# Performance work log

Hardware: AMD Instinct MI355X
Metric: run time of the kernel (lower is better)

## Reference

```python
import jax, jax.numpy as jnp
import numpy as np

B, DIM, N = 4, 256, 2048
DIM_CTX, M = 256, 2048
HEADS, DIM_HEAD = 8, 64
DIM_INNER = HEADS * DIM_HEAD  # 512
EPS = 1e-12  # matches F.normalize eps


def setup_inputs() -> dict:
    key = jax.random.key(0)
    ks = jax.random.split(key, 8)
    return {
        "fmap": jax.random.normal(ks[0], (B, DIM, N), dtype=jnp.float32),
        "context": jax.random.normal(ks[1], (B, DIM_CTX, M), dtype=jnp.float32),
        "mask": jax.random.randint(ks[2], (B, M), 0, 2) > 0,
        "gamma": jnp.ones((DIM, 1), dtype=jnp.float32),
        "gamma_ctx": jnp.ones((DIM_CTX, 1), dtype=jnp.float32),
        "Wq": jax.random.normal(ks[3], (DIM_INNER, DIM), dtype=jnp.float32) * (DIM ** -0.5),
        "Wkv": jax.random.normal(ks[4], (2 * DIM_INNER, DIM_CTX), dtype=jnp.float32) * (DIM_CTX ** -0.5),
        "Wout": jax.random.normal(ks[5], (DIM, DIM_INNER), dtype=jnp.float32) * (DIM_INNER ** -0.5),
    }


def channel_rmsnorm(x, gamma):
    # F.normalize(x, dim=1) * sqrt(dim) * gamma ; x: [b, c, n], gamma: [c, 1]
    scale = x.shape[1] ** 0.5
    norm = jnp.sqrt(jnp.sum(x * x, axis=1, keepdims=True))
    normed = x / jnp.maximum(norm, EPS)
    return normed * scale * gamma[None]


def reference(fmap, context, mask, gamma, gamma_ctx, Wq, Wkv, Wout):
    h, d = HEADS, DIM_HEAD
    attn_scale = d ** -0.5

    fmap_n = channel_rmsnorm(fmap, gamma)          # [b, dim, n]
    ctx_n = channel_rmsnorm(context, gamma_ctx)    # [b, dim_ctx, m]

    # 1x1 Conv1d == matmul over channels
    q = jnp.einsum('oc,bcn->bon', Wq, fmap_n)      # [b, h*d, n]
    kv = jnp.einsum('oc,bcm->bom', Wkv, ctx_n)     # [b, 2*h*d, m]
    k, v = jnp.split(kv, 2, axis=1)

    # [b, h*d, n] -> [b, h, n, d]
    def to_heads(t):
        b, _, nn = t.shape
        return t.reshape(b, h, d, nn).transpose(0, 1, 3, 2)

    q, k, v = to_heads(q), to_heads(k), to_heads(v)

    # L2-distance attention: sim = -||q_i - k_j||_2 * scale
    q2 = jnp.sum(q * q, axis=-1)                   # [b, h, n]
    k2 = jnp.sum(k * k, axis=-1)                   # [b, h, m]
    qk = jnp.einsum('bhid,bhjd->bhij', q, k)       # [b, h, n, m]
    d2 = jnp.maximum(q2[..., :, None] + k2[..., None, :] - 2.0 * qk, 0.0)
    dist = jnp.sqrt(jnp.maximum(d2, EPS))
    sim = -dist * attn_scale

    neg_max = -jnp.finfo(sim.dtype).max
    sim = jnp.where(mask[:, None, None, :], sim, neg_max)

    attn = jax.nn.softmax(sim, axis=-1)            # [b, h, n, m]
    out = jnp.einsum('bhij,bhjd->bhid', attn, v)   # [b, h, n, d]
    out = out.transpose(0, 1, 3, 2).reshape(out.shape[0], h * d, -1)  # [b, h*d, n]
    return jnp.einsum('oc,bcn->bon', Wout, out)    # [b, dim, n]
```

## Files before the change

kernel.cpp:

```cpp
#include <hip/hip_runtime.h>
#include <hip/hip_bf16.h>

#define B_ 4
#define DIM_ 256
#define N_ 2048
#define M_ 2048
#define HEADS_ 8
#define DHEAD_ 64
#define DINNER_ 512

typedef __attribute__((ext_vector_type(8))) short short8;
typedef __attribute__((ext_vector_type(4))) short short4v;
typedef __attribute__((ext_vector_type(4))) float floatx4;
typedef __attribute__((ext_vector_type(4))) _Float16 half4;
typedef __attribute__((ext_vector_type(8))) _Float16 half8;

#if defined(__has_builtin)
#if __has_builtin(__builtin_amdgcn_global_load_lds)
#define HAS_DMA 1
#endif
#endif

typedef __attribute__((address_space(1))) const void gvoid_t;
typedef __attribute__((address_space(3))) void lvoid_t;

#define CQ_ 0.18033688011112042f
#define NEG2CQ_ (-0.36067376022224084f)
#define EPS2_ 3.25213893e-14f

__device__ inline short bf16r(float x) {
  unsigned u = __float_as_uint(x);
  unsigned r = (u + 0x7fffu + ((u >> 16) & 1u)) >> 16;
  return (short)r;
}
__device__ inline float bf2f(short b) {
  return __uint_as_float(((unsigned)(unsigned short)b) << 16);
}

__global__ __launch_bounds__(256) void wsplit_kernel(
    const float* __restrict__ Wq, const float* __restrict__ Wkv,
    const float* __restrict__ Wout, const float* __restrict__ gamma,
    const float* __restrict__ gctx, short* __restrict__ whi,
    short* __restrict__ wlo) {
  const int y = blockIdx.y;
  const int gsz[3] = {32768, 65536, 32768};
  const int goff[3] = {0, 131072, 393216};
  int gidx = blockIdx.x * 256 + threadIdx.x;
  if (gidx >= gsz[y]) return;
  const float* W = (y == 0) ? Wq : (y == 1) ? Wkv : Wout;
  const int cmask = (y == 2) ? 511 : 255;
  int e0 = gidx * 4;
  int c = e0 & cmask;
  float4 wv = *(const float4*)&W[e0];
  if (y < 2) {
    const float* g = (y == 0) ? gamma : gctx;
    float4 g4 = *(const float4*)&g[c];
    wv.x *= g4.x; wv.y *= g4.y; wv.z *= g4.z; wv.w *= g4.w;
  }
  float vv[4] = {wv.x, wv.y, wv.z, wv.w};
  short4v hi, lo;
#pragma unroll
  for (int e = 0; e < 4; ++e) {
    short hb = bf16r(vv[e]);
    hi[e] = hb;
    lo[e] = bf16r(vv[e] - bf2f(hb));
  }
  *(short4v*)&whi[goff[y] + e0] = hi;
  *(short4v*)&wlo[goff[y] + e0] = lo;
}

__global__ __launch_bounds__(256) void colnorm_t_kernel(
    const float* __restrict__ xf, const float* __restrict__ xc,
    short* __restrict__ xtf, short* __restrict__ xtc, int NN) {
  const float* x = (blockIdx.z == 0) ? xf : xc;
  short* xt = (blockIdx.z == 0) ? xtf : xtc;
  int b = blockIdx.y;
  int tx = threadIdx.x, ty = threadIdx.y;
  int n0 = blockIdx.x * 64, n = n0 + tx;
  const float* xb = x + (size_t)b * 256 * NN;

  float ssq = 0.f;
  for (int c = ty; c < 256; c += 4) {
    float v = xb[(size_t)c * NN + n];
    ssq += v * v;
  }
  __shared__ float red[4][64];
  __shared__ float scl[64];
  __shared__ float t[64][65];
  red[ty][tx] = ssq;
  __syncthreads();
  if (ty == 0) {
    float s = red[0][tx] + red[1][tx] + red[2][tx] + red[3][tx];
    scl[tx] = 16.0f / fmaxf(sqrtf(s), 1e-12f);
  }
  int tid = ty * 64 + tx;
  int row = tid >> 2, cg = tid & 3;
  for (int c0 = 0; c0 < 256; c0 += 64) {
    __syncthreads();
    for (int cc = ty; cc < 64; cc += 4) t[cc][tx] = xb[(size_t)(c0 + cc) * NN + n];
    __syncthreads();
    float sc = scl[row];
    short8 o0v, o1v;
#pragma unroll
    for (int e = 0; e < 8; ++e) {
      o0v[e] = bf16r(t[cg * 16 + e][row] * sc);
      o1v[e] = bf16r(t[cg * 16 + 8 + e][row] * sc);
    }
    size_t base = ((size_t)b * NN + n0 + row) * 256 + c0 + cg * 16;
    *(short8*)&xt[base] = o0v;
    *(short8*)&xt[base + 8] = o1v;
  }
}

__global__ __launch_bounds__(256) void qkv_gemm_kernel(
    const short* __restrict__ whi, const short* __restrict__ wlo,
    const short* __restrict__ fmap_t, const short* __restrict__ ctx_t,
    short* __restrict__ qb, short* __restrict__ kc, _Float16* __restrict__ vc,
    const int* __restrict__ maskp, float* __restrict__ k2m) {
  const int b = blockIdx.z;
  const int y = blockIdx.y;
  const bool isq = (y < 4);
  const int o0 = (isq ? y : y - 4) * 128;
  const int n0 = blockIdx.x * 128;
  const short* Wh = whi + (isq ? 0 : 131072);
  const short* Wl = wlo + (isq ? 0 : 131072);
  const short* Xt = isq ? fmap_t : ctx_t;

  const int tid = threadIdx.x;
  const int w = tid >> 6, l = tid & 63, quad = l >> 4, l15 = l & 15;
  const int wo = (w >> 1) * 64, wn = (w & 1) * 64;

  __shared__ __align__(16) short Wa[2][128][40];
  __shared__ __align__(16) short Xb[128][40];

  floatx4 acc[4][4];
#pragma unroll
  for (int ot = 0; ot < 4; ++ot)
#pragma unroll
    for (int nt = 0; nt < 4; ++nt)
#pragma unroll
      for (int r = 0; r < 4; ++r) acc[ot][nt][r] = 0.f;

  for (int c0 = 0; c0 < 256; c0 += 32) {
    __syncthreads();
#pragma unroll
    for (int it = 0; it < 2; ++it) {
      int lin = tid + it * 256;
      int row = lin >> 2, sg = (lin & 3) * 8;
      size_t src = (size_t)(o0 + row) * 256 + c0 + sg;
      *(short8*)&Wa[0][row][sg] = *(const short8*)&Wh[src];
      *(short8*)&Wa[1][row][sg] = *(const short8*)&Wl[src];
    }
#pragma unroll
    for (int it = 0; it < 2; ++it) {
      int lin = tid + it * 256;
      int nn = lin >> 2, sg = (lin & 3) * 8;
      *(short8*)&Xb[nn][sg] =
          *(const short8*)&Xt[((size_t)b * 2048 + n0 + nn) * 256 + c0 + sg];
    }
    __syncthreads();

    short8 ah[4], al[4], bx[4];
#pragma unroll
    for (int ot = 0; ot < 4; ++ot) {
      ah[ot] = *(const short8*)&Wa[0][wo + 16 * ot + l15][8 * quad];
      al[ot] = *(const short8*)&Wa[1][wo + 16 * ot + l15][8 * quad];
    }
#pragma unroll
    for (int nt = 0; nt < 4; ++nt)
      bx[nt] = *(const short8*)&Xb[wn + 16 * nt + l15][8 * quad];
#pragma unroll
    for (int ot = 0; ot < 4; ++ot)
#pragma unroll
      for (int nt = 0; nt < 4; ++nt) {
        acc[ot][nt] =
            __builtin_amdgcn_mfma_f32_16x16x32_bf16(al[ot], bx[nt], acc[ot][nt], 0, 0, 0);
        acc[ot][nt] =
            __builtin_amdgcn_mfma_f32_16x16x32_bf16(ah[ot], bx[nt], acc[ot][nt], 0, 0, 0);
      }
  }

  if (isq) {
#pragma unroll
    for (int nt = 0; nt < 4; ++nt) {
      int n = n0 + wn + 16 * nt + l15;
      size_t base = ((size_t)b * 2048 + n) * 512;
#pragma unroll
      for (int ot = 0; ot < 4; ++ot) {
        int o = o0 + wo + 16 * ot + 4 * quad;
        short4v pk;
#pragma unroll
        for (int r = 0; r < 4; ++r) pk[r] = bf16r(CQ_ * acc[ot][nt][r]);
        *(short4v*)&qb[base + o] = pk;
      }
    }
  } else if (o0 < 512) {
    const int head = (o0 + wo) >> 6;
    const int bh = b * 8 + head;
    float k2p[4] = {0.f, 0.f, 0.f, 0.f};
#pragma unroll
    for (int nt = 0; nt < 4; ++nt) {
      int m = n0 + wn + 16 * nt + l15;
      int chunk = m >> 6, mrow = m & 63;
      size_t tbase = (((size_t)bh * 32 + chunk) * 64 + mrow) * 64;
      int sw = mrow & 7;
#pragma unroll
      for (int ot = 0; ot < 4; ++ot) {
        int d0 = 16 * ot + 4 * quad;
        short4v pk;
#pragma unroll
        for (int r = 0; r < 4; ++r) {
          short pv = bf16r(NEG2CQ_ * acc[ot][nt][r]);
          pk[r] = pv;
          float kr = bf2f(pv);
          k2p[nt] += kr * kr;
        }
        *(short4v*)&kc[tbase + (size_t)(((d0 >> 3) ^ sw) << 3) + (d0 & 7)] = pk;
      }
    }
#pragma unroll
    for (int nt = 0; nt < 4; ++nt) {
      float s = k2p[nt];
      s += __shfl_xor(s, 16);
      s += __shfl_xor(s, 32);
      if (quad == 0) {
        int m = n0 + wn + 16 * nt + l15;
        int mv = maskp[b * 2048 + m];
        k2m[(size_t)bh * 2048 + m] = mv ? 0.25f * s : __builtin_inff();
      }
    }
  } else {
    const int chv = o0 - 512 + wo;
    const int bh = b * 8 + (chv >> 6);
#pragma unroll
    for (int nt = 0; nt < 4; ++nt) {
      int j = n0 + wn + 16 * nt + l15;
      int chunk = j >> 6, jr = j & 63;
      int jrem = jr & 31;
      int colp = 32 * (jr >> 5) + ((jrem >> 2) & 3) * 8 + (jrem >> 4) * 4 +
                 (jrem & 3);
      size_t cbase = ((size_t)bh * 32 + chunk) * 4096;
#pragma unroll
      for (int ot = 0; ot < 4; ++ot)
#pragma unroll
        for (int r = 0; r < 4; ++r) {
          int drow = (chv + 16 * ot + 4 * quad + r) & 63;
          vc[cbase + drow * 64 + (((colp >> 3) ^ (drow & 7)) << 3) +
             (colp & 7)] = (_Float16)acc[ot][nt][r];
        }
    }
  }
}

__global__ __launch_bounds__(512, 8) void attn_kernel(
    const short* __restrict__ qb, const short* __restrict__ kc,
    const _Float16* __restrict__ vc, const float* __restrict__ k2m,
    short* __restrict__ attn_t) {
  const int bid = blockIdx.x;
  const int rr = bid & 7, qq = bid >> 3;
  const int bh = rr * 4 + (qq >> 5);
  const int iblk = qq & 31;
  const int h = bh & 7, b = bh >> 3;
  const int i0 = iblk * 64;

  const int tid = threadIdx.x;
  const int w = tid >> 6, l = tid & 63, quad = l >> 4, l15 = l & 15;
  const int wr = w >> 1, jh = w & 1;

  __shared__ __align__(16) short sbuf[2][2][4096];

  const short* qrow =
      qb + ((size_t)b * 2048 + i0 + 16 * wr + l15) * 512 + h * 64;
  const short* kcb = kc + (size_t)bh * 32 * 4096;
  const _Float16* vcb = vc + (size_t)bh * 32 * 4096;
  const float* k2b = k2m + (size_t)bh * 2048;

  short8 qa0 = *(const short8*)&qrow[8 * quad];
  short8 qa1 = *(const short8*)&qrow[32 + 8 * quad];
  float q2p = 0.f;
#pragma unroll
  for (int jj = 0; jj < 8; ++jj) {
    float f0 = bf2f(qa0[jj]), f1 = bf2f(qa1[jj]);
    q2p += f0 * f0 + f1 * f1;
  }
  q2p += __shfl_xor(q2p, 16);
  q2p += __shfl_xor(q2p, 32);
  const float q2c = q2p;

  floatx4 accO[4];
#pragma unroll
  for (int dt = 0; dt < 4; ++dt)
#pragma unroll
    for (int r = 0; r < 4; ++r) accO[dt][r] = 0.f;
  float lsum = 0.f;

  const int sx = l15 & 7;

  auto stage = [&](int c, int p) {
    const short* ks = kcb + (size_t)c * 4096 + w * 512 + l * 8;
    const _Float16* vs = vcb + (size_t)c * 4096 + w * 512 + l * 8;
#ifdef HAS_DMA
    __builtin_amdgcn_global_load_lds((gvoid_t*)ks,
                                     (lvoid_t*)&sbuf[0][p][w * 512], 16, 0, 0);
    __builtin_amdgcn_global_load_lds((gvoid_t*)vs,
                                     (lvoid_t*)&sbuf[1][p][w * 512], 16, 0, 0);
#else
    *(short8*)&sbuf[0][p][w * 512 + l * 8] = *(const short8*)ks;
    *(half8*)&((_Float16*)sbuf[1][p])[w * 512 + l * 8] = *(const half8*)vs;
#endif
  };

  stage(0, 0);
  for (int c = 0; c < 32; ++c) {
    __syncthreads();
    if (c < 31) stage(c + 1, (c + 1) & 1);
    const int p = c & 1;

    half4 pb0, pb1;
#pragma unroll
    for (int jt = 0; jt < 2; ++jt) {
      float4 k2v = *(const float4*)&k2b[c * 64 + jh * 32 + 16 * jt + 4 * quad];
      const short* kr = &sbuf[0][p][(jh * 32 + 16 * jt + l15) * 64];
      short8 k0 = *(const short8*)&kr[(quad ^ sx) << 3];
      short8 k1 = *(const short8*)&kr[((quad + 4) ^ sx) << 3];
      floatx4 a;
      a[0] = q2c + k2v.x;
      a[1] = q2c + k2v.y;
      a[2] = q2c + k2v.z;
      a[3] = q2c + k2v.w;
      __builtin_amdgcn_s_setprio(1);
      a = __builtin_amdgcn_mfma_f32_16x16x32_bf16(k0, qa0, a, 0, 0, 0);
      a = __builtin_amdgcn_mfma_f32_16x16x32_bf16(k1, qa1, a, 0, 0, 0);
      __builtin_amdgcn_s_setprio(0);
      half4 pbt;
#pragma unroll
      for (int r = 0; r < 4; ++r) {
        float s = __builtin_amdgcn_sqrtf(fmaxf(a[r], EPS2_));
        float pv = __builtin_amdgcn_exp2f(-s);
        lsum += pv;
        pbt[r] = (_Float16)pv;
      }
      if (jt == 0) pb0 = pbt; else pb1 = pbt;
    }

    __builtin_amdgcn_s_setprio(1);
#pragma unroll
    for (int dt = 0; dt < 4; ++dt) {
      const _Float16* vr = (const _Float16*)&sbuf[1][p][(16 * dt + l15) * 64];
      half8 hh = *(const half8*)&vr[((quad + 4 * jh) ^ sx) << 3];
      half4 vaA = __builtin_shufflevector(hh, hh, 0, 1, 2, 3);
      half4 vaB = __builtin_shufflevector(hh, hh, 4, 5, 6, 7);
      accO[dt] = __builtin_amdgcn_mfma_f32_16x16x16f16(vaA, pb0, accO[dt], 0, 0, 0);
      accO[dt] = __builtin_amdgcn_mfma_f32_16x16x16f16(vaB, pb1, accO[dt], 0, 0, 0);
    }
    __builtin_amdgcn_s_setprio(0);
  }

  __syncthreads();
  float* scr = (float*)sbuf;
  const int sidx = (wr * 64 + l) * 17;
  if (jh) {
#pragma unroll
    for (int dt = 0; dt < 4; ++dt)
#pragma unroll
      for (int r = 0; r < 4; ++r) scr[sidx + dt * 4 + r] = accO[dt][r];
    scr[sidx + 16] = lsum;
  }
  __syncthreads();
  if (!jh) {
#pragma unroll
    for (int dt = 0; dt < 4; ++dt)
#pragma unroll
      for (int r = 0; r < 4; ++r) accO[dt][r] += scr[sidx + dt * 4 + r];
    lsum += scr[sidx + 16];
    lsum += __shfl_xor(lsum, 16);
    lsum += __shfl_xor(lsum, 32);
    float rl = 1.0f / lsum;
    size_t base = ((size_t)b * 2048 + i0 + 16 * wr + l15) * 512 + h * 64;
#pragma unroll
    for (int dt = 0; dt < 4; ++dt) {
      short4v pk;
#pragma unroll
      for (int r = 0; r < 4; ++r) pk[r] = bf16r(accO[dt][r] * rl);
      *(short4v*)&attn_t[base + 16 * dt + 4 * quad] = pk;
    }
  }
}

__global__ __launch_bounds__(256) void outproj_kernel(
    const short* __restrict__ whi, const short* __restrict__ wlo,
    const short* __restrict__ Xt, float* __restrict__ Yf) {
  const int b = blockIdx.z;
  const int n0 = blockIdx.x * 128;
  const int o0 = blockIdx.y * 64;
  const int tid = threadIdx.x;
  const int w = tid >> 6, l = tid & 63, quad = l >> 4, l15 = l & 15;
  const int wo = (w >> 1) * 32, wn = (w & 1) * 64;

  __shared__ __align__(16) short Wa[2][64][40];
  __shared__ __align__(16) short Xb[128][40];

  floatx4 acc[2][4];
#pragma unroll
  for (int ot = 0; ot < 2; ++ot)
#pragma unroll
    for (int nt = 0; nt < 4; ++nt)
#pragma unroll
      for (int r = 0; r < 4; ++r) acc[ot][nt][r] = 0.f;

  for (int c0 = 0; c0 < 512; c0 += 32) {
    __syncthreads();
    {
      int row = tid >> 2, sg = (tid & 3) * 8;
      size_t src = (size_t)(o0 + row) * 512 + c0 + sg;
      *(short8*)&Wa[0][row][sg] = *(const short8*)&whi[src];
      *(short8*)&Wa[1][row][sg] = *(const short8*)&wlo[src];
    }
#pragma unroll
    for (int it = 0; it < 2; ++it) {
      int lin = tid + it * 256;
      int nn = lin >> 2, sg = (lin & 3) * 8;
      *(short8*)&Xb[nn][sg] =
          *(const short8*)&Xt[((size_t)b * 2048 + n0 + nn) * 512 + c0 + sg];
    }
    __syncthreads();

    short8 ah[2], al[2], bx[4];
#pragma unroll
    for (int ot = 0; ot < 2; ++ot) {
      ah[ot] = *(const short8*)&Wa[0][wo + 16 * ot + l15][8 * quad];
      al[ot] = *(const short8*)&Wa[1][wo + 16 * ot + l15][8 * quad];
    }
#pragma unroll
    for (int nt = 0; nt < 4; ++nt)
      bx[nt] = *(const short8*)&Xb[wn + 16 * nt + l15][8 * quad];
#pragma unroll
    for (int ot = 0; ot < 2; ++ot)
#pragma unroll
      for (int nt = 0; nt < 4; ++nt) {
        acc[ot][nt] =
            __builtin_amdgcn_mfma_f32_16x16x32_bf16(al[ot], bx[nt], acc[ot][nt], 0, 0, 0);
        acc[ot][nt] =
            __builtin_amdgcn_mfma_f32_16x16x32_bf16(ah[ot], bx[nt], acc[ot][nt], 0, 0, 0);
      }
  }

#pragma unroll
  for (int ot = 0; ot < 2; ++ot)
#pragma unroll
    for (int r = 0; r < 4; ++r) {
      int o = o0 + wo + 16 * ot + 4 * quad + r;
#pragma unroll
      for (int nt = 0; nt < 4; ++nt)
        Yf[((size_t)b * 256 + o) * 2048 + n0 + wn + 16 * nt + l15] =
            acc[ot][nt][r];
    }
}

extern "C" void kernel_launch(void* const* d_in, const int* in_sizes, int n_in,
                              void* d_out, int out_size, void* d_ws,
                              size_t ws_size, hipStream_t stream) {
  const float* fmap = (const float*)d_in[0];
  const float* context = (const float*)d_in[1];
  const int* mask = (const int*)d_in[2];
  const float* gamma = (const float*)d_in[3];
  const float* gamma_ctx = (const float*)d_in[4];
  const float* Wq = (const float*)d_in[5];
  const float* Wkv = (const float*)d_in[6];
  const float* Wout = (const float*)d_in[7];
  float* out = (float*)d_out;

  char* ws = (char*)d_ws;
  short* fmap_t = (short*)ws;
  short* ctx_t = fmap_t + 2097152;
  short* qb = ctx_t + 2097152;
  short* kc = qb + 4194304;
  _Float16* vc = (_Float16*)(kc + 4194304);
  short* attn_t = (short*)(vc + 4194304);
  float* k2m = (float*)(attn_t + 4194304);
  short* whi = (short*)(k2m + 65536);
  short* wlo = whi + 524288;

  dim3 blk64x4(64, 4);
  wsplit_kernel<<<dim3(256, 3), 256, 0, stream>>>(Wq, Wkv, Wout, gamma,
                                                  gamma_ctx, whi, wlo);
  colnorm_t_kernel<<<dim3(32, B_, 2), blk64x4, 0, stream>>>(
      fmap, context, fmap_t, ctx_t, N_);
  qkv_gemm_kernel<<<dim3(16, 12, B_), 256, 0, stream>>>(
      whi, wlo, fmap_t, ctx_t, qb, kc, vc, mask, k2m);
  attn_kernel<<<dim3(1024), 512, 0, stream>>>(qb, kc, vc, k2m, attn_t);
  outproj_kernel<<<dim3(16, 4, B_), 256, 0, stream>>>(whi + 393216,
                                                      wlo + 393216, attn_t,
                                                      out);
}
```

Before: 209.6 us.

## Software-pipeline attention loop: overlap P·V of previous tile with QK of current

Restructures the attention main loop so that the P·V MFMAs for the previous key tile run in the same iteration as the QK MFMAs for the current tile. The softmax probabilities are carried across iterations, and V staging is delayed by one stage. The change also prefetches the k2 norms one tile ahead in registers, and merges the two 16x16x16 f16 MFMAs into a single 16x16x32 f16 MFMA. The intent is to hide the sqrt/exp latency and LDS waits behind independent matrix work. In exchange it adds register pressure and an epilogue step for the final tile.

```diff
diff --git a/kernel.cpp b/kernel.cpp
--- a/kernel.cpp
+++ b/kernel.cpp
@@ -267,7 +267,8 @@
   const int w = tid >> 6, l = tid & 63, quad = l >> 4, l15 = l & 15;
   const int wr = w >> 1, jh = w & 1;
 
-  __shared__ __align__(16) short sbuf[2][2][4096];
+  __shared__ __align__(16) short kbuf[2][4096];
+  __shared__ __align__(16) short vbuf[2][4096];
 
   const short* qrow =
       qb + ((size_t)b * 2048 + i0 + 16 * wr + l15) * 512 + h * 64;
@@ -292,87 +293,120 @@
   for (int dt = 0; dt < 4; ++dt)
 #pragma unroll
     for (int r = 0; r < 4; ++r) accO[dt][r] = 0.f;
-  float lsum = 0.f;
+  float lsum0 = 0.f, lsum1 = 0.f;
 
   const int sx = l15 & 7;
 
-  auto stage = [&](int c, int p) {
+  auto stageK = [&](int c, int p) {
     const short* ks = kcb + (size_t)c * 4096 + w * 512 + l * 8;
+#ifdef HAS_DMA
+    __builtin_amdgcn_global_load_lds((gvoid_t*)ks,
+                                     (lvoid_t*)&kbuf[p][w * 512], 16, 0, 0);
+#else
+    *(short8*)&kbuf[p][w * 512 + l * 8] = *(const short8*)ks;
+#endif
+  };
+  auto stageV = [&](int c, int p) {
     const _Float16* vs = vcb + (size_t)c * 4096 + w * 512 + l * 8;
 #ifdef HAS_DMA
-    __builtin_amdgcn_global_load_lds((gvoid_t*)ks,
-                                     (lvoid_t*)&sbuf[0][p][w * 512], 16, 0, 0);
     __builtin_amdgcn_global_load_lds((gvoid_t*)vs,
-                                     (lvoid_t*)&sbuf[1][p][w * 512], 16, 0, 0);
+                                     (lvoid_t*)&vbuf[p][w * 512], 16, 0, 0);
 #else
-    *(short8*)&sbuf[0][p][w * 512 + l * 8] = *(const short8*)ks;
-    *(half8*)&((_Float16*)sbuf[1][p])[w * 512 + l * 8] = *(const half8*)vs;
+    *(half8*)&((_Float16*)vbuf[p])[w * 512 + l * 8] = *(const half8*)vs;
 #endif
   };
 
-  stage(0, 0);
+  float4 k2pf0 = *(const float4*)&k2b[jh * 32 + 4 * quad];
+  float4 k2pf1 = *(const float4*)&k2b[jh * 32 + 16 + 4 * quad];
+
+  stageK(0, 0);
+  half8 pbprev;
   for (int c = 0; c < 32; ++c) {
     __syncthreads();
-    if (c < 31) stage(c + 1, (c + 1) & 1);
     const int p = c & 1;
-
-    half4 pb0, pb1;
-#pragma unroll
-    for (int jt = 0; jt < 2; ++jt) {
-      float4 k2v = *(const float4*)&k2b[c * 64 + jh * 32 + 16 * jt + 4 * quad];
-      const short* kr = &sbuf[0][p][(jh * 32 + 16 * jt + l15) * 64];
-      short8 k0 = *(const short8*)&kr[(quad ^ sx) << 3];
-      short8 k1 = *(const short8*)&kr[((quad + 4) ^ sx) << 3];
-      floatx4 a;
-      a[0] = q2c + k2v.x;
-      a[1] = q2c + k2v.y;
-      a[2] = q2c + k2v.z;
-      a[3] = q2c + k2v.w;
-      __builtin_amdgcn_s_setprio(1);
-      a = __builtin_amdgcn_mfma_f32_16x16x32_bf16(k0, qa0, a, 0, 0, 0);
-      a = __builtin_amdgcn_mfma_f32_16x16x32_bf16(k1, qa1, a, 0, 0, 0);
-      __builtin_amdgcn_s_setprio(0);
-      half4 pbt;
-#pragma unroll
-      for (int r = 0; r < 4; ++r) {
-        float s = __builtin_amdgcn_sqrtf(fmaxf(a[r], EPS2_));
-        float pv = __builtin_amdgcn_exp2f(-s);
-        lsum += pv;
-        pbt[r] = (_Float16)pv;
+    if (c < 31) stageK(c + 1, p ^ 1);
+    stageV(c, p);
+
+    float4 k2c0 = k2pf0, k2c1 = k2pf1;
+    if (c < 31) {
+      k2pf0 = *(const float4*)&k2b[(c + 1) * 64 + jh * 32 + 4 * quad];
+      k2pf1 = *(const float4*)&k2b[(c + 1) * 64 + jh * 32 + 16 + 4 * quad];
+    }
+
+    const short* kr0 = &kbuf[p][(jh * 32 + l15) * 64];
+    const short* kr1 = &kbuf[p][(jh * 32 + 16 + l15) * 64];
+    short8 k00 = *(const short8*)&kr0[(quad ^ sx) << 3];
+    short8 k01 = *(const short8*)&kr0[((quad + 4) ^ sx) << 3];
+    short8 k10 = *(const short8*)&kr1[(quad ^ sx) << 3];
+    short8 k11 = *(const short8*)&kr1[((quad + 4) ^ sx) << 3];
+
+    floatx4 a0, a1;
+    a0[0] = q2c + k2c0.x; a0[1] = q2c + k2c0.y;
+    a0[2] = q2c + k2c0.z; a0[3] = q2c + k2c0.w;
+    a1[0] = q2c + k2c1.x; a1[1] = q2c + k2c1.y;
+    a1[2] = q2c + k2c1.z; a1[3] = q2c + k2c1.w;
+
+    __builtin_amdgcn_s_setprio(1);
+    a0 = __builtin_amdgcn_mfma_f32_16x16x32_bf16(k00, qa0, a0, 0, 0, 0);
+    a0 = __builtin_amdgcn_mfma_f32_16x16x32_bf16(k01, qa1, a0, 0, 0, 0);
+    a1 = __builtin_amdgcn_mfma_f32_16x16x32_bf16(k10, qa0, a1, 0, 0, 0);
+    a1 = __builtin_amdgcn_mfma_f32_16x16x32_bf16(k11, qa1, a1, 0, 0, 0);
+    if (c > 0) {
+#pragma unroll
+      for (int dt = 0; dt < 4; ++dt) {
+        const _Float16* vr = (const _Float16*)&vbuf[p ^ 1][(16 * dt + l15) * 64];
+        half8 hh = *(const half8*)&vr[((quad + 4 * jh) ^ sx) << 3];
+        accO[dt] =
+            __builtin_amdgcn_mfma_f32_16x16x32_f16(hh, pbprev, accO[dt], 0, 0, 0);
       }
-      if (jt == 0) pb0 = pbt; else pb1 = pbt;
-    }
-
-    __builtin_amdgcn_s_setprio(1);
-#pragma unroll
-    for (int dt = 0; dt < 4; ++dt) {
-      const _Float16* vr = (const _Float16*)&sbuf[1][p][(16 * dt + l15) * 64];
-      half8 hh = *(const half8*)&vr[((quad + 4 * jh) ^ sx) << 3];
-      half4 vaA = __builtin_shufflevector(hh, hh, 0, 1, 2, 3);
-      half4 vaB = __builtin_shufflevector(hh, hh, 4, 5, 6, 7);
-      accO[dt] = __builtin_amdgcn_mfma_f32_16x16x16f16(vaA, pb0, accO[dt], 0, 0, 0);
-      accO[dt] = __builtin_amdgcn_mfma_f32_16x16x16f16(vaB, pb1, accO[dt], 0, 0, 0);
     }
     __builtin_amdgcn_s_setprio(0);
+
+    half8 pbc;
+#pragma unroll
+    for (int r = 0; r < 4; ++r) {
+      float s = __builtin_amdgcn_sqrtf(fmaxf(a0[r], EPS2_));
+      float pv = __builtin_amdgcn_exp2f(-s);
+      lsum0 += pv;
+      pbc[r] = (_Float16)pv;
+    }
+#pragma unroll
+    for (int r = 0; r < 4; ++r) {
+      float s = __builtin_amdgcn_sqrtf(fmaxf(a1[r], EPS2_));
+      float pv = __builtin_amdgcn_exp2f(-s);
+      lsum1 += pv;
+      pbc[4 + r] = (_Float16)pv;
+    }
+    pbprev = pbc;
   }
 
   __syncthreads();
-  float* scr = (float*)sbuf;
-  const int sidx = (wr * 64 + l) * 17;
+#pragma unroll
+  for (int dt = 0; dt < 4; ++dt) {
+    const _Float16* vr = (const _Float16*)&vbuf[1][(16 * dt + l15) * 64];
+    half8 hh = *(const half8*)&vr[((quad + 4 * jh) ^ sx) << 3];
+    accO[dt] =
+        __builtin_amdgcn_mfma_f32_16x16x32_f16(hh, pbprev, accO[dt], 0, 0, 0);
+  }
+  float lsum = lsum0 + lsum1;
+
+  float* scrO = (float*)kbuf;
+  float* scrL = (float*)vbuf;
+  const int sidx = wr * 64 + l;
   if (jh) {
 #pragma unroll
     for (int dt = 0; dt < 4; ++dt)
 #pragma unroll
-      for (int r = 0; r < 4; ++r) scr[sidx + dt * 4 + r] = accO[dt][r];
-    scr[sidx + 16] = lsum;
+      for (int r = 0; r < 4; ++r) scrO[sidx * 16 + dt * 4 + r] = accO[dt][r];
+    scrL[sidx] = lsum;
   }
   __syncthreads();
   if (!jh) {
 #pragma unroll
     for (int dt = 0; dt < 4; ++dt)
 #pragma unroll
-      for (int r = 0; r < 4; ++r) accO[dt][r] += scr[sidx + dt * 4 + r];
-    lsum += scr[sidx + 16];
+      for (int r = 0; r < 4; ++r) accO[dt][r] += scrO[sidx * 16 + dt * 4 + r];
+    lsum += scrL[sidx];
     lsum += __shfl_xor(lsum, 16);
     lsum += __shfl_xor(lsum, 32);
     float rl = 1.0f / lsum;
```

Result: slower. 352.7 us (+68.3%).
